# Optimization experiments

Hardware: AMD Instinct MI355X
Metric: run time of the kernel (lower is better)

Reference implementation:

```python
import jax, jax.numpy as jnp
import numpy as np

N_NODES = 8192
N_EDGES = 65536
NB = 10            # number_of_basis
MID = 32           # middle_layer_size
MAX_R = 10.0       # max_radius
NZ, NM = 48, 16    # z / mol embedding sizes -> 64x0e node input
IN_S = NZ + NM     # 64 scalars
H_S, H_V = 32, 8   # hidden irreps 32x0e + 8x1o (dim 56)
O_S = 16           # output irreps 16x0e
W0N = IN_S * H_S + IN_S * H_V                                  # 2560
W1N = H_S*H_S + H_V*H_S + H_S*H_V + H_V*H_V + H_V*H_V          # 1664
W2N = H_S*O_S + H_V*O_S                                        # 640
H_DIM = H_S + 3 * H_V                                          # 56


def _fcnet(e, W1, W2):
    # e3nn FullyConnectedNet([NB, MID, numel], silu): fan-in normalized linears
    h = jax.nn.silu(e @ W1 / np.sqrt(W1.shape[0]))
    return h @ W2 / np.sqrt(W2.shape[0])


def _ln(x, g, b):
    m = jnp.mean(x, -1, keepdims=True)
    v = jnp.var(x, -1, keepdims=True)
    return (x - m) * jax.lax.rsqrt(v + 1e-5) * g + b


def _sus(t):
    # smooth compact-support bump helper: exp(-1/t) for t>0 else 0
    return jnp.where(t > 0, jnp.exp(-1.0 / jnp.where(t > 0, t, 1.0)), 0.0)


def _forward(pos, Ez, Em,
             b0_W1, b0_W2, b0_g, b0_b,
             b1_W1, b1_W2, b1_g, b1_b,
             b2_W1, b2_W2, b2_g, b2_b,
             z, mol_id, edge_src, edge_dst):
    N = pos.shape[0]
    E = edge_src.shape[0]
    avg = E / N  # avg_num_neighbors (static)

    # node embedding: 64x0e
    x = jnp.concatenate([Ez[z], Em[mol_id]], axis=-1)          # [N, 64]

    vec = pos[edge_dst] - pos[edge_src]                        # [E, 3]
    length = jnp.linalg.norm(vec, axis=1)                      # [E]

    # soft_one_hot_linspace(basis='smooth_finite', cutoff=True) * sqrt(NB)
    vals = jnp.linspace(0.0, MAX_R, NB + 2)[1:-1]
    step = MAX_R / (NB + 1)
    u = (length[:, None] - vals) / step
    emb = (1.14136 * np.exp(2.0)) * _sus(u + 1.0) * _sus(1.0 - u)
    emb = emb * np.sqrt(NB)                                    # [E, NB]

    # spherical harmonics lmax=1, normalize=True, 'component' norm
    nrm = vec / jnp.maximum(length, 1e-9)[:, None]
    sh_v = np.sqrt(3.0) * nrm                                  # [E, 3]  (l=1; l=0 comp == 1)

    # ---- interaction block 0: 64x0e -> 32x0e + 8x1o ----
    w = _fcnet(emb, b0_W1, b0_W2)                              # [E, 2560]
    w00 = w[:, :IN_S * H_S].reshape(E, IN_S, H_S)
    w01 = w[:, IN_S * H_S:].reshape(E, IN_S, H_V)
    xe = x[edge_src]                                           # [E, 64]
    es = jnp.einsum('eu,euw->ew', xe, w00) / np.sqrt(IN_S)
    ev = jnp.einsum('eu,euw,ei->ewi', xe, w01, sh_v) / np.sqrt(IN_S)
    msg = jnp.concatenate([es, ev.reshape(E, 3 * H_V)], -1)    # [E, 56]
    x = _ln(jax.ops.segment_sum(msg, edge_dst, num_segments=N) / np.sqrt(avg), b0_g, b0_b)

    # ---- interaction block 1: 32x0e+8x1o -> 32x0e+8x1o ----
    w = _fcnet(emb, b1_W1, b1_W2)                              # [E, 1664]
    o = 0
    w_ss  = w[:, o:o + H_S*H_S].reshape(E, H_S, H_S); o += H_S*H_S
    w_vvs = w[:, o:o + H_V*H_S].reshape(E, H_V, H_S); o += H_V*H_S
    w_sv  = w[:, o:o + H_S*H_V].reshape(E, H_S, H_V); o += H_S*H_V
    w_vs  = w[:, o:o + H_V*H_V].reshape(E, H_V, H_V); o += H_V*H_V
    w_vvv = w[:, o:o + H_V*H_V].reshape(E, H_V, H_V)
    xs = x[:, :H_S][edge_src]                                  # [E, 32]
    xv = x[:, H_S:].reshape(N, H_V, 3)[edge_src]               # [E, 8, 3]
    dot = jnp.einsum('eui,ei->eu', xv, sh_v) / np.sqrt(3.0)    # 1o x 1o -> 0e CG
    crs = jnp.cross(xv, sh_v[:, None, :]) / np.sqrt(2.0)       # 1o x 1o -> 1o CG
    es = (jnp.einsum('eu,euw->ew', xs, w_ss) / np.sqrt(H_S)
          + jnp.einsum('eu,euw->ew', dot, w_vvs) / np.sqrt(H_V)) / np.sqrt(2.0)
    ev = (jnp.einsum('eu,euw,ei->ewi', xs, w_sv, sh_v) / np.sqrt(H_S)
          + jnp.einsum('eui,euw->ewi', xv, w_vs) / np.sqrt(H_V)
          + jnp.einsum('eui,euw->ewi', crs, w_vvv) / np.sqrt(H_V)) / np.sqrt(3.0)
    msg = jnp.concatenate([es, ev.reshape(E, 3 * H_V)], -1)
    x = _ln(jax.ops.segment_sum(msg, edge_dst, num_segments=N) / np.sqrt(avg), b1_g, b1_b)

    # ---- interaction block 2: 32x0e+8x1o -> 16x0e ----
    w = _fcnet(emb, b2_W1, b2_W2)                              # [E, 640]
    w_ss  = w[:, :H_S * O_S].reshape(E, H_S, O_S)
    w_vvs = w[:, H_S * O_S:].reshape(E, H_V, O_S)
    xs = x[:, :H_S][edge_src]
    xv = x[:, H_S:].reshape(N, H_V, 3)[edge_src]
    dot = jnp.einsum('eui,ei->eu', xv, sh_v) / np.sqrt(3.0)
    es = (jnp.einsum('eu,euw->ew', xs, w_ss) / np.sqrt(H_S)
          + jnp.einsum('eu,euw->ew', dot, w_vvs) / np.sqrt(H_V)) / np.sqrt(2.0)
    x = _ln(jax.ops.segment_sum(es, edge_dst, num_segments=N) / np.sqrt(avg), b2_g, b2_b)
    return x                                                   # [N, 16]


def setup_inputs():
    key = jax.random.key(0)
    ks = jax.random.split(key, 16)
    edge_src = jax.random.randint(ks[3], (N_EDGES,), 0, N_NODES)
    # exclude self-loops (radius_graph never returns them)
    edge_dst = (edge_src + 1 + jax.random.randint(ks[4], (N_EDGES,), 0, N_NODES - 1)) % N_NODES
    return {
        'pos': jax.random.uniform(ks[0], (N_NODES, 3), jnp.float32) * 8.0,
        'z': jax.random.randint(ks[1], (N_NODES,), 0, 100),
        'mol_id': jax.random.randint(ks[2], (N_NODES,), 0, 2),
        'edge_src': edge_src,
        'edge_dst': edge_dst,
        'Ez': jax.random.normal(ks[5], (100, NZ), jnp.float32),
        'Em': jax.random.normal(ks[6], (2, NM), jnp.float32),
        'b0_W1': jax.random.normal(ks[7], (NB, MID), jnp.float32),
        'b0_W2': jax.random.normal(ks[8], (MID, W0N), jnp.float32),
        'b0_g': jnp.ones((H_DIM,), jnp.float32),
        'b0_b': jnp.zeros((H_DIM,), jnp.float32),
        'b1_W1': jax.random.normal(ks[9], (NB, MID), jnp.float32),
        'b1_W2': jax.random.normal(ks[10], (MID, W1N), jnp.float32),
        'b1_g': jnp.ones((H_DIM,), jnp.float32),
        'b1_b': jnp.zeros((H_DIM,), jnp.float32),
        'b2_W1': jax.random.normal(ks[11], (NB, MID), jnp.float32),
        'b2_W2': jax.random.normal(ks[12], (MID, W2N), jnp.float32),
        'b2_g': jnp.ones((O_S,), jnp.float32),
        'b2_b': jnp.zeros((O_S,), jnp.float32),
    }


def reference(pos, z, mol_id, edge_src, edge_dst, Ez, Em,
              b0_W1, b0_W2, b0_g, b0_b,
              b1_W1, b1_W2, b1_g, b1_b,
              b2_W1, b2_W2, b2_g, b2_b):
    return _forward(pos, Ez, Em,
                    b0_W1, b0_W2, b0_g, b0_b,
                    b1_W1, b1_W2, b1_g, b1_b,
                    b2_W1, b2_W2, b2_g, b2_b,
                    z, mol_id, edge_src, edge_dst)
```

## Files before the change

### kernel.cpp

```cpp
#include <hip/hip_runtime.h>

#define NNODES 8192
#define NEDGES 65536

#define K_PACK   0.02209708691f
#define K_P1SV   0.01804219593f
#define K_VVS    0.04419417382f
#define K_VS     0.03608439182f
#define K_VVV    0.02551551815f
#define K_DOT    0.57735026919f
#define K_PRELN  0.35355339059f
#define C_EMB    8.4335730689f

typedef unsigned int uint32;
typedef unsigned short ushort16;
typedef __attribute__((ext_vector_type(8))) short short8;
typedef __attribute__((ext_vector_type(4))) float floatx4;

__device__ __forceinline__ float siluf(float x) { return x / (1.0f + __expf(-x)); }
__device__ __forceinline__ float susf(float t) { return t > 0.0f ? __expf(-1.0f / t) : 0.0f; }
__device__ __forceinline__ ushort16 f2bf(float f) {
  uint32 u = __float_as_uint(f);
  return (ushort16)((u + 0x7fffu + ((u >> 16) & 1u)) >> 16);
}
__device__ __forceinline__ float bflo(uint32 v) { return __uint_as_float(v << 16); }
__device__ __forceinline__ float bfhi(uint32 v) { return __uint_as_float(v & 0xffff0000u); }
__device__ __forceinline__ float bfs(ushort16 v) { return __uint_as_float((uint32)v << 16); }

__global__ __launch_bounds__(256) void k_prep(
    const float* __restrict__ pos, const int* __restrict__ z, const int* __restrict__ mol,
    const int* __restrict__ esrc, const int* __restrict__ edst,
    const float* __restrict__ Ez, const float* __restrict__ Em,
    const float* __restrict__ W10, const float* __restrict__ W11, const float* __restrict__ W12,
    const float* __restrict__ W20, const float* __restrict__ W21, const float* __restrict__ W22,
    int* __restrict__ combo, ushort16* __restrict__ X0cb, float* __restrict__ sh,
    ushort16* __restrict__ h0b, ushort16* __restrict__ h1b, ushort16* __restrict__ h2b,
    ushort16* __restrict__ Bp0, ushort16* __restrict__ Bp1, ushort16* __restrict__ Bp2,
    ushort16* __restrict__ Bpw1, ushort16* __restrict__ Bpw2,
    int* __restrict__ deg, int* __restrict__ eidx) {
  __shared__ float Wl[320];
  int b = blockIdx.x;
  if (b < 768) {
    int which = b >> 8;
    int e = ((b & 255) << 8) + threadIdx.x;
    const float* W = (which == 0) ? W10 : (which == 1) ? W11 : W12;
    for (int i = threadIdx.x; i < 320; i += 256) Wl[i] = W[i];
    __syncthreads();
    int s = esrc[e], d = edst[e];
    float vx = pos[d * 3 + 0] - pos[s * 3 + 0];
    float vy = pos[d * 3 + 1] - pos[s * 3 + 1];
    float vz = pos[d * 3 + 2] - pos[s * 3 + 2];
    float len = sqrtf(vx * vx + vy * vy + vz * vz);
    if (which == 0) {
      int p = atomicAdd(&deg[d], 1);
      if (p < 64) eidx[(size_t)d * 64 + p] = e;
      float inv = 1.7320508076f / fmaxf(len, 1e-9f);
      sh[e * 3 + 0] = vx * inv; sh[e * 3 + 1] = vy * inv; sh[e * 3 + 2] = vz * inv;
    }
    float emb[10];
#pragma unroll
    for (int k = 0; k < 10; ++k) {
      float u = len * 1.1f - (float)(k + 1);
      emb[k] = C_EMB * susf(u + 1.0f) * susf(1.0f - u);
    }
    float H[32];
#pragma unroll
    for (int m = 0; m < 32; ++m) {
      float t = 0.f;
#pragma unroll
      for (int k = 0; k < 10; ++k) t += emb[k] * Wl[k * 32 + m];
      H[m] = siluf(t);
    }
    ushort16* hb = (which == 0) ? h0b : (which == 1) ? h1b : h2b;
    uint32* hp = (uint32*)(hb + (size_t)e * 32);
#pragma unroll
    for (int m = 0; m < 16; ++m)
      hp[m] = (uint32)f2bf(H[2 * m]) | ((uint32)f2bf(H[2 * m + 1]) << 16);
    return;
  }
  int idx = (b - 768) * 256 + threadIdx.x;
  if (idx < NNODES) { combo[idx] = z[idx] * 2 + mol[idx]; return; }
  idx -= NNODES;
  if (idx < 16384) {
    int c = idx >> 6, j = idx & 63;
    float v = 0.f;
    if (c < 200) {
      int zz = c >> 1, mm = c & 1;
      v = (j < 48) ? Ez[zz * 48 + j] : Em[mm * 16 + (j - 48)];
    }
    X0cb[idx] = f2bf(v);
    return;
  }
  idx -= 16384;
  if (idx < 81920) {
    int tile = idx >> 10; int r = idx & 1023;
    int kh = r >> 9; int rr = r & 511;
    int lane = rr >> 3, j = rr & 7;
    int k = kh * 32 + (lane >> 4) * 8 + j;
    int n = tile * 16 + (lane & 15);
    int c = n >> 5, m = n & 31;
    int col = (c < 32) ? (k * 32 + c) : (2048 + k * 8 + (c - 32));
    Bp0[idx] = f2bf(W20[m * 2560 + col] * K_PACK);
    return;
  }
  idx -= 81920;
  if (idx < 40960) {
    int tile = idx >> 9; int rr = idx & 511;
    int lane = rr >> 3, j = rr & 7;
    int k = (lane >> 4) * 8 + j;
    int n = tile * 16 + (lane & 15);
    int c = n >> 5, m = n & 31;
    float v = (c < 32) ? W21[m * 1664 + k * 32 + c] * K_PACK
                       : W21[m * 1664 + 1280 + k * 8 + (c - 32)] * K_P1SV;
    Bp1[idx] = f2bf(v);
    return;
  }
  idx -= 40960;
  if (idx < 16384) {
    int tile = idx >> 9; int rr = idx & 511;
    int lane = rr >> 3, j = rr & 7;
    int k = (lane >> 4) * 8 + j;
    int n = tile * 16 + (lane & 15);
    int c = n >> 5, m = n & 31;
    Bp2[idx] = f2bf(W22[m * 640 + k * 16 + c] * K_PACK);
    return;
  }
  idx -= 16384;
  if (idx < 12288) {
    int tile = idx >> 9; int rr = idx & 511;
    int lane = rr >> 3, j = rr & 7;
    int m = (lane >> 4) * 8 + j;
    int c = tile * 16 + (lane & 15);
    float v;
    if (c < 256) {
      int u = c >> 5, w = c & 31;
      v = W21[m * 1664 + 1024 + u * 32 + w] * K_VVS;
    } else {
      int r2 = c - 256; int t = r2 & 1; int l2 = r2 >> 1;
      int u = l2 >> 3, vv = l2 & 7;
      v = (t == 0) ? W21[m * 1664 + 1536 + u * 8 + vv] * K_VS
                   : W21[m * 1664 + 1600 + u * 8 + vv] * K_VVV;
    }
    Bpw1[idx] = f2bf(v);
    return;
  }
  idx -= 12288;
  {
    int tile = idx >> 9; int rr = idx & 511;
    int lane = rr >> 3, j = rr & 7;
    int m = (lane >> 4) * 8 + j;
    int c = tile * 16 + (lane & 15);
    int t = c & 1; int l2 = c >> 1;
    int u = l2 >> 3, wh = l2 & 7;
    Bpw2[idx] = f2bf(W22[m * 640 + 512 + u * 16 + wh * 2 + t] * K_VVS);
  }
}

__device__ __forceinline__ void gemm_tile(
    const ushort16* __restrict__ A, const ushort16* __restrict__ Bp, ushort16* __restrict__ C,
    int N, int K, int bx, int by, int wave, int lane) {
  int m0 = bx * 64 + wave * 16;
  int n0 = by * 64;
  int row = lane & 15, q = lane >> 4;
  int nkh = K >> 5;
  floatx4 acc[4];
  floatx4 zero = {0.f, 0.f, 0.f, 0.f};
#pragma unroll
  for (int t = 0; t < 4; ++t) acc[t] = zero;
  for (int kh = 0; kh < nkh; ++kh) {
    short8 a = *reinterpret_cast<const short8*>(A + (size_t)(m0 + row) * K + kh * 32 + q * 8);
#pragma unroll
    for (int t = 0; t < 4; ++t) {
      int T = (n0 >> 4) + t;
      short8 b = *reinterpret_cast<const short8*>(Bp + ((size_t)T * nkh + kh) * 512 + lane * 8);
      acc[t] = __builtin_amdgcn_mfma_f32_16x16x32_bf16(a, b, acc[t], 0, 0, 0);
    }
  }
  int colb = n0 + row;
#pragma unroll
  for (int t = 0; t < 4; ++t)
#pragma unroll
    for (int r = 0; r < 4; ++r)
      C[(size_t)(m0 + q * 4 + r) * N + colb + t * 16] = f2bf(acc[t][r]);
}

__global__ __launch_bounds__(256) void k_gemm_mfma(
    const ushort16* __restrict__ A, const ushort16* __restrict__ Bp, ushort16* __restrict__ C,
    int N, int K) {
  gemm_tile(A, Bp, C, N, K, blockIdx.x, blockIdx.y, threadIdx.x >> 6, threadIdx.x & 63);
}

__global__ __launch_bounds__(256) void k_msg0(
    const int* __restrict__ rowmap, const int* __restrict__ esrc,
    const float* __restrict__ sh, const ushort16* __restrict__ hb,
    const ushort16* __restrict__ Pb, ushort16* __restrict__ msg) {
  int e = __builtin_amdgcn_readfirstlane(blockIdx.x * 4 + (threadIdx.x >> 6));
  int lane = threadIdx.x & 63;
  int s = esrc[e];
  int row = rowmap[s];
  float sh0 = sh[e * 3 + 0], sh1 = sh[e * 3 + 1], sh2 = sh[e * 3 + 2];
  int c; float mult;
  if (lane < 32) { c = lane; mult = 1.0f; }
  else if (lane < 56) {
    int l = lane - 32; int v = l / 3; int i = l - v * 3;
    c = 32 + v;
    mult = (i == 0) ? sh0 : (i == 1 ? sh1 : sh2);
  } else { c = 0; mult = 0.0f; }
  const uint4* Hp = reinterpret_cast<const uint4*>(hb + (size_t)e * 32);
  const uint4* Pp = reinterpret_cast<const uint4*>(Pb + (size_t)row * 1280 + c * 32);
  float a = 0.f;
#pragma unroll
  for (int qq = 0; qq < 4; ++qq) {
    uint4 pv = Pp[qq];
    uint4 hv = Hp[qq];
    a += bflo(pv.x) * bflo(hv.x) + bfhi(pv.x) * bfhi(hv.x);
    a += bflo(pv.y) * bflo(hv.y) + bfhi(pv.y) * bfhi(hv.y);
    a += bflo(pv.z) * bflo(hv.z) + bfhi(pv.z) * bfhi(hv.z);
    a += bflo(pv.w) * bflo(hv.w) + bfhi(pv.w) * bfhi(hv.w);
  }
  if (lane < 56) msg[(size_t)e * 56 + lane] = f2bf(a * mult);
}

__global__ __launch_bounds__(256) void k_msg1f(
    const int* __restrict__ esrc, const float* __restrict__ sh, const ushort16* __restrict__ hb,
    const ushort16* __restrict__ Pb, const float* __restrict__ xv,
    const ushort16* __restrict__ Bpw, ushort16* __restrict__ msg) {
  __shared__ ushort16 Wlds[16][384];
  __shared__ float vbuf[4][56];
  int w = threadIdx.x >> 6, lane = threadIdx.x & 63;
  int e0 = __builtin_amdgcn_readfirstlane(blockIdx.x * 16);
  int row = lane & 15, q = lane >> 4;
  short8 a1 = *reinterpret_cast<const short8*>(hb + (size_t)(e0 + row) * 32 + q * 8);
  floatx4 zero = {0.f, 0.f, 0.f, 0.f};
#pragma unroll
  for (int t6 = 0; t6 < 6; ++t6) {
    int T = w * 6 + t6;
    short8 b1 = *reinterpret_cast<const short8*>(Bpw + (size_t)T * 512 + lane * 8);
    floatx4 acc = __builtin_amdgcn_mfma_f32_16x16x32_bf16(a1, b1, zero, 0, 0, 0);
#pragma unroll
    for (int r = 0; r < 4; ++r)
      Wlds[q * 4 + r][T * 16 + row] = f2bf(acc[r]);
  }
  __syncthreads();
  int u = lane >> 3;
#pragma unroll
  for (int k = 0; k < 4; ++k) {
    int e = e0 + w * 4 + k;
    int s = esrc[e];
    float sh0 = sh[e * 3 + 0], sh1 = sh[e * 3 + 1], sh2 = sh[e * 3 + 2];
    const float* xvp = xv + (size_t)s * 24 + u * 3;
    float x0 = xvp[0], x1 = xvp[1], x2 = xvp[2];
    float du = K_DOT * (x0 * sh0 + x1 * sh1 + x2 * sh2);
    float cr0 = x1 * sh2 - x2 * sh1;
    float cr1 = x2 * sh0 - x0 * sh2;
    float cr2 = x0 * sh1 - x1 * sh0;
    const ushort16* wp = &Wlds[w * 4 + k][0];
    uint2 wv = *reinterpret_cast<const uint2*>(wp + lane * 4);
    uint32 wsv = *reinterpret_cast<const uint32*>(wp + 256 + lane * 2);
    float b0 = du * bflo(wv.x), b1 = du * bfhi(wv.x);
    float b2 = du * bflo(wv.y), b3 = du * bfhi(wv.y);
    float avs = bflo(wsv), avv = bfhi(wsv);
    float e0v = x0 * avs + cr0 * avv;
    float e1v = x1 * avs + cr1 * avv;
    float e2v = x2 * avs + cr2 * avv;
#pragma unroll
    for (int off = 8; off < 64; off <<= 1) {
      b0 += __shfl_xor(b0, off, 64); b1 += __shfl_xor(b1, off, 64);
      b2 += __shfl_xor(b2, off, 64); b3 += __shfl_xor(b3, off, 64);
      e0v += __shfl_xor(e0v, off, 64); e1v += __shfl_xor(e1v, off, 64);
      e2v += __shfl_xor(e2v, off, 64);
    }
    if (lane < 8) {
      vbuf[w][lane * 4 + 0] = b0; vbuf[w][lane * 4 + 1] = b1;
      vbuf[w][lane * 4 + 2] = b2; vbuf[w][lane * 4 + 3] = b3;
      vbuf[w][32 + lane * 3 + 0] = e0v;
      vbuf[w][32 + lane * 3 + 1] = e1v;
      vbuf[w][32 + lane * 3 + 2] = e2v;
    }
    int c; float mult;
    if (lane < 32) { c = lane; mult = 1.0f; }
    else if (lane < 56) {
      int l = lane - 32; int v = l / 3; int i = l - v * 3;
      c = 32 + v;
      mult = (i == 0) ? sh0 : (i == 1 ? sh1 : sh2);
    } else { c = 0; mult = 0.0f; }
    const uint4* Hp = reinterpret_cast<const uint4*>(hb + (size_t)e * 32);
    const uint4* Pp = reinterpret_cast<const uint4*>(Pb + (size_t)s * 1280 + c * 32);
    float a = 0.f;
#pragma unroll
    for (int qq = 0; qq < 4; ++qq) {
      uint4 pv = Pp[qq];
      uint4 hv = Hp[qq];
      a += bflo(pv.x) * bflo(hv.x) + bfhi(pv.x) * bfhi(hv.x);
      a += bflo(pv.y) * bflo(hv.y) + bfhi(pv.y) * bfhi(hv.y);
      a += bflo(pv.z) * bflo(hv.z) + bfhi(pv.z) * bfhi(hv.z);
      a += bflo(pv.w) * bflo(hv.w) + bfhi(pv.w) * bfhi(hv.w);
    }
    __syncthreads();
    if (lane < 56) msg[(size_t)e * 56 + lane] = f2bf(a * mult + vbuf[w][lane]);
  }
}

__global__ __launch_bounds__(256) void k_msg2f(
    const int* __restrict__ esrc, const float* __restrict__ sh, const ushort16* __restrict__ hb,
    const ushort16* __restrict__ Pb, const float* __restrict__ xv,
    const ushort16* __restrict__ Bpw, ushort16* __restrict__ msg) {
  __shared__ ushort16 Wlds[16][128];
  __shared__ float vbuf[4][16];
  int w = threadIdx.x >> 6, lane = threadIdx.x & 63;
  int e0 = __builtin_amdgcn_readfirstlane(blockIdx.x * 16);
  int row = lane & 15, q = lane >> 4;
  short8 a1 = *reinterpret_cast<const short8*>(hb + (size_t)(e0 + row) * 32 + q * 8);
  floatx4 zero = {0.f, 0.f, 0.f, 0.f};
#pragma unroll
  for (int t2 = 0; t2 < 2; ++t2) {
    int T = w * 2 + t2;
    short8 b1 = *reinterpret_cast<const short8*>(Bpw + (size_t)T * 512 + lane * 8);
    floatx4 acc = __builtin_amdgcn_mfma_f32_16x16x32_bf16(a1, b1, zero, 0, 0, 0);
#pragma unroll
    for (int r = 0; r < 4; ++r)
      Wlds[q * 4 + r][T * 16 + row] = f2bf(acc[r]);
  }
  __syncthreads();
  int u = lane >> 3;
#pragma unroll
  for (int k = 0; k < 4; ++k) {
    int e = e0 + w * 4 + k;
    int s = esrc[e];
    float sh0 = sh[e * 3 + 0], sh1 = sh[e * 3 + 1], sh2 = sh[e * 3 + 2];
    const float* xvp = xv + (size_t)s * 24 + u * 3;
    float du = K_DOT * (xvp[0] * sh0 + xvp[1] * sh1 + xvp[2] * sh2);
    uint32 w2 = *reinterpret_cast<const uint32*>(&Wlds[w * 4 + k][0] + lane * 2);
    float c0 = du * bflo(w2), c1 = du * bfhi(w2);
#pragma unroll
    for (int off = 8; off < 64; off <<= 1) {
      c0 += __shfl_xor(c0, off, 64); c1 += __shfl_xor(c1, off, 64);
    }
    if (lane < 8) { vbuf[w][lane * 2 + 0] = c0; vbuf[w][lane * 2 + 1] = c1; }
    int qq = lane >> 4, wc = lane & 15;
    uint4 hv = reinterpret_cast<const uint4*>(hb + (size_t)e * 32)[qq];
    uint4 pv = reinterpret_cast<const uint4*>(Pb + (size_t)s * 512 + wc * 32)[qq];
    float a = bflo(pv.x) * bflo(hv.x) + bfhi(pv.x) * bfhi(hv.x)
            + bflo(pv.y) * bflo(hv.y) + bfhi(pv.y) * bfhi(hv.y)
            + bflo(pv.z) * bflo(hv.z) + bfhi(pv.z) * bfhi(hv.z)
            + bflo(pv.w) * bflo(hv.w) + bfhi(pv.w) * bfhi(hv.w);
    a += __shfl_xor(a, 16, 64);
    a += __shfl_xor(a, 32, 64);
    __syncthreads();
    if (lane < 16) msg[(size_t)e * 16 + lane] = f2bf(a + vbuf[w][lane]);
  }
}

__global__ __launch_bounds__(256) void k_gather_ln(
    const int* __restrict__ deg, const int* __restrict__ eidx,
    const ushort16* __restrict__ msg, int D,
    const float* __restrict__ g, const float* __restrict__ b,
    ushort16* __restrict__ xsb, float* __restrict__ xvf, float* __restrict__ outf) {
  int n = __builtin_amdgcn_readfirstlane(blockIdx.x * 4 + (threadIdx.x >> 6));
  int lane = threadIdx.x & 63;
  int cnt = deg[n]; if (cnt > 64) cnt = 64;
  const int* ep = eidx + (size_t)n * 64;
  float v = 0.f;
  for (int j = 0; j < cnt; ++j) {
    int e = ep[j];
    if (lane < D) v += bfs(msg[(size_t)e * D + lane]);
  }
  v *= K_PRELN;
  if (lane >= D) v = 0.f;
  float sm = v, sq = v * v;
#pragma unroll
  for (int off = 32; off > 0; off >>= 1) {
    sm += __shfl_xor(sm, off, 64);
    sq += __shfl_xor(sq, off, 64);
  }
  float invD = 1.0f / (float)D;
  float mean = sm * invD;
  float var = sq * invD - mean * mean;
  float rs = rsqrtf(var + 1e-5f);
  float r = (v - mean) * rs * g[lane < D ? lane : 0] + b[lane < D ? lane : 0];
  if (outf) {
    if (lane < D) outf[(size_t)n * D + lane] = r;
  } else {
    if (lane < 32) xsb[(size_t)n * 32 + lane] = f2bf(r);
    else if (lane < 56) xvf[(size_t)n * 24 + lane - 32] = r;
  }
}

extern "C" void kernel_launch(void* const* d_in, const int* in_sizes, int n_in,
                              void* d_out, int out_size, void* d_ws, size_t ws_size,
                              hipStream_t stream) {
  const float* pos = (const float*)d_in[0];
  const int* z = (const int*)d_in[1];
  const int* mol = (const int*)d_in[2];
  const int* esrc = (const int*)d_in[3];
  const int* edst = (const int*)d_in[4];
  const float* Ez = (const float*)d_in[5];
  const float* Em = (const float*)d_in[6];
  const float* b0W1 = (const float*)d_in[7];
  const float* b0W2 = (const float*)d_in[8];
  const float* b0g = (const float*)d_in[9];
  const float* b0b = (const float*)d_in[10];
  const float* b1W1 = (const float*)d_in[11];
  const float* b1W2 = (const float*)d_in[12];
  const float* b1g = (const float*)d_in[13];
  const float* b1b = (const float*)d_in[14];
  const float* b2W1 = (const float*)d_in[15];
  const float* b2W2 = (const float*)d_in[16];
  const float* b2g = (const float*)d_in[17];
  const float* b2b = (const float*)d_in[18];
  float* out = (float*)d_out;

  float* ws = (float*)d_ws;
  size_t o = 0;
  int* combo = (int*)(ws + o); o += NNODES;
  int* deg = (int*)(ws + o); o += NNODES;
  int* eidx = (int*)(ws + o); o += (size_t)NNODES * 64;
  ushort16* X0cb = (ushort16*)(ws + o); o += 8192;
  ushort16* xs1b = (ushort16*)(ws + o); o += 131072;
  float* xv1 = ws + o; o += (size_t)NNODES * 24;
  ushort16* h0b = (ushort16*)(ws + o); o += (size_t)NEDGES * 16;
  ushort16* h1b = (ushort16*)(ws + o); o += (size_t)NEDGES * 16;
  ushort16* h2b = (ushort16*)(ws + o); o += (size_t)NEDGES * 16;
  float* shb = ws + o; o += (size_t)NEDGES * 3;
  ushort16* Bp0 = (ushort16*)(ws + o); o += 40960;
  ushort16* Bp1 = (ushort16*)(ws + o); o += 20480;
  ushort16* Bp2 = (ushort16*)(ws + o); o += 8192;
  ushort16* Bpw1 = (ushort16*)(ws + o); o += 6144;
  ushort16* Bpw2 = (ushort16*)(ws + o); o += 2048;
  ushort16* P12 = (ushort16*)(ws + o); o += (size_t)NNODES * 640;
  ushort16* msgb = (ushort16*)(ws + o); o += (size_t)NEDGES * 28;

  ushort16* P0c = P12;
  ushort16* xs2b = xs1b;
  float* xv2 = xv1;
  ushort16* msg16 = msgb;

  hipMemsetAsync(deg, 0, NNODES * sizeof(int), stream);

  k_prep<<<1472, 256, 0, stream>>>(pos, z, mol, esrc, edst, Ez, Em,
                                   b0W1, b1W1, b2W1, b0W2, b1W2, b2W2,
                                   combo, X0cb, shb, h0b, h1b, h2b,
                                   Bp0, Bp1, Bp2, Bpw1, Bpw2, deg, eidx);

  k_gemm_mfma<<<dim3(4, 20), 256, 0, stream>>>(X0cb, Bp0, P0c, 1280, 64);
  k_msg0<<<16384, 256, 0, stream>>>(combo, esrc, shb, h0b, P0c, msgb);
  k_gather_ln<<<2048, 256, 0, stream>>>(deg, eidx, msgb, 56, b0g, b0b, xs1b, xv1, nullptr);

  k_gemm_mfma<<<dim3(128, 20), 256, 0, stream>>>(xs1b, Bp1, P12, 1280, 32);
  k_msg1f<<<4096, 256, 0, stream>>>(esrc, shb, h1b, P12, xv1, Bpw1, msgb);
  k_gather_ln<<<2048, 256, 0, stream>>>(deg, eidx, msgb, 56, b1g, b1b, xs2b, xv2, nullptr);

  k_gemm_mfma<<<dim3(128, 8), 256, 0, stream>>>(xs2b, Bp2, P12, 512, 32);
  k_msg2f<<<4096, 256, 0, stream>>>(esrc, shb, h2b, P12, xv2, Bpw2, msg16);
  k_gather_ln<<<2048, 256, 0, stream>>>(deg, eidx, msg16, 16, b2g, b2b, nullptr, nullptr, out);
}
```

Before: 225.0 us.

## Process edges in source-sorted order for message kernels with block swizzle

Counts out-degree per source node, scans it into row pointers (fused into the first GEMM launch), and builds a source-sorted edge permutation during k_msg0. k_msg1f and k_msg2f then walk edges in that permuted order, so consecutive edges share the same source-node P rows and xv data. They also use a block-index swizzle. The aim is better L2 locality for the per-source gathers. The cost is extra atomics, a scan and indirect edge indexing. Messages are still written by original edge id, so the gather stage is unchanged.

```diff
diff --git a/kernel.cpp b/kernel.cpp
--- a/kernel.cpp
+++ b/kernel.cpp
@@ -37,7 +37,7 @@
     ushort16* __restrict__ h0b, ushort16* __restrict__ h1b, ushort16* __restrict__ h2b,
     ushort16* __restrict__ Bp0, ushort16* __restrict__ Bp1, ushort16* __restrict__ Bp2,
     ushort16* __restrict__ Bpw1, ushort16* __restrict__ Bpw2,
-    int* __restrict__ deg, int* __restrict__ eidx) {
+    int* __restrict__ deg, int* __restrict__ deg_s, int* __restrict__ eidx) {
   __shared__ float Wl[320];
   int b = blockIdx.x;
   if (b < 768) {
@@ -54,6 +54,7 @@
     if (which == 0) {
       int p = atomicAdd(&deg[d], 1);
       if (p < 64) eidx[(size_t)d * 64 + p] = e;
+      atomicAdd(&deg_s[s], 1);
       float inv = 1.7320508076f / fmaxf(len, 1e-9f);
       sh[e * 3 + 0] = vx * inv; sh[e * 3 + 1] = vy * inv; sh[e * 3 + 2] = vz * inv;
     }
@@ -190,13 +191,47 @@
   gemm_tile(A, Bp, C, N, K, blockIdx.x, blockIdx.y, threadIdx.x >> 6, threadIdx.x & 63);
 }
 
+__global__ __launch_bounds__(256) void k_gemm_scan(
+    const ushort16* __restrict__ A, const ushort16* __restrict__ Bp, ushort16* __restrict__ C,
+    const int* __restrict__ deg_s, int* __restrict__ rowptr_s) {
+  __shared__ int sums[256];
+  int b = blockIdx.x;
+  if (b < 80) {
+    gemm_tile(A, Bp, C, 1280, 64, b % 4, b / 4, threadIdx.x >> 6, threadIdx.x & 63);
+    return;
+  }
+  int t = threadIdx.x;
+  int base = t * 32;
+  int local[32];
+  int s = 0;
+#pragma unroll
+  for (int i = 0; i < 32; ++i) { local[i] = s; s += deg_s[base + i]; }
+  sums[t] = s;
+  __syncthreads();
+  for (int off = 1; off < 256; off <<= 1) {
+    int v = (t >= off) ? sums[t - off] : 0;
+    __syncthreads();
+    sums[t] += v;
+    __syncthreads();
+  }
+  int prev = (t == 0) ? 0 : sums[t - 1];
+#pragma unroll
+  for (int i = 0; i < 32; ++i) rowptr_s[base + i] = prev + local[i];
+  if (t == 255) rowptr_s[NNODES] = sums[255];
+}
+
 __global__ __launch_bounds__(256) void k_msg0(
     const int* __restrict__ rowmap, const int* __restrict__ esrc,
     const float* __restrict__ sh, const ushort16* __restrict__ hb,
-    const ushort16* __restrict__ Pb, ushort16* __restrict__ msg) {
+    const ushort16* __restrict__ Pb, ushort16* __restrict__ msg,
+    const int* __restrict__ rowptr_s, int* __restrict__ fill_s, int* __restrict__ eperm) {
   int e = __builtin_amdgcn_readfirstlane(blockIdx.x * 4 + (threadIdx.x >> 6));
   int lane = threadIdx.x & 63;
   int s = esrc[e];
+  if (lane == 0) {
+    int p = atomicAdd(&fill_s[s], 1);
+    eperm[rowptr_s[s] + p] = e;
+  }
   int row = rowmap[s];
   float sh0 = sh[e * 3 + 0], sh1 = sh[e * 3 + 1], sh2 = sh[e * 3 + 2];
   int c; float mult;
@@ -222,15 +257,19 @@
 }
 
 __global__ __launch_bounds__(256) void k_msg1f(
-    const int* __restrict__ esrc, const float* __restrict__ sh, const ushort16* __restrict__ hb,
+    const int* __restrict__ eperm, const int* __restrict__ esrc,
+    const float* __restrict__ sh, const ushort16* __restrict__ hb,
     const ushort16* __restrict__ Pb, const float* __restrict__ xv,
     const ushort16* __restrict__ Bpw, ushort16* __restrict__ msg) {
   __shared__ ushort16 Wlds[16][384];
   __shared__ float vbuf[4][56];
   int w = threadIdx.x >> 6, lane = threadIdx.x & 63;
-  int e0 = __builtin_amdgcn_readfirstlane(blockIdx.x * 16);
+  int bid = blockIdx.x;
+  int swz = (bid & 7) * 512 + (bid >> 3);
+  int e0 = __builtin_amdgcn_readfirstlane(swz * 16);
   int row = lane & 15, q = lane >> 4;
-  short8 a1 = *reinterpret_cast<const short8*>(hb + (size_t)(e0 + row) * 32 + q * 8);
+  int er = eperm[e0 + row];
+  short8 a1 = *reinterpret_cast<const short8*>(hb + (size_t)er * 32 + q * 8);
   floatx4 zero = {0.f, 0.f, 0.f, 0.f};
 #pragma unroll
   for (int t6 = 0; t6 < 6; ++t6) {
@@ -245,7 +284,7 @@
   int u = lane >> 3;
 #pragma unroll
   for (int k = 0; k < 4; ++k) {
-    int e = e0 + w * 4 + k;
+    int e = __builtin_amdgcn_readfirstlane(eperm[e0 + w * 4 + k]);
     int s = esrc[e];
     float sh0 = sh[e * 3 + 0], sh1 = sh[e * 3 + 1], sh2 = sh[e * 3 + 2];
     const float* xvp = xv + (size_t)s * 24 + u * 3;
@@ -302,15 +341,19 @@
 }
 
 __global__ __launch_bounds__(256) void k_msg2f(
-    const int* __restrict__ esrc, const float* __restrict__ sh, const ushort16* __restrict__ hb,
+    const int* __restrict__ eperm, const int* __restrict__ esrc,
+    const float* __restrict__ sh, const ushort16* __restrict__ hb,
     const ushort16* __restrict__ Pb, const float* __restrict__ xv,
     const ushort16* __restrict__ Bpw, ushort16* __restrict__ msg) {
   __shared__ ushort16 Wlds[16][128];
   __shared__ float vbuf[4][16];
   int w = threadIdx.x >> 6, lane = threadIdx.x & 63;
-  int e0 = __builtin_amdgcn_readfirstlane(blockIdx.x * 16);
+  int bid = blockIdx.x;
+  int swz = (bid & 7) * 512 + (bid >> 3);
+  int e0 = __builtin_amdgcn_readfirstlane(swz * 16);
   int row = lane & 15, q = lane >> 4;
-  short8 a1 = *reinterpret_cast<const short8*>(hb + (size_t)(e0 + row) * 32 + q * 8);
+  int er = eperm[e0 + row];
+  short8 a1 = *reinterpret_cast<const short8*>(hb + (size_t)er * 32 + q * 8);
   floatx4 zero = {0.f, 0.f, 0.f, 0.f};
 #pragma unroll
   for (int t2 = 0; t2 < 2; ++t2) {
@@ -325,7 +368,7 @@
   int u = lane >> 3;
 #pragma unroll
   for (int k = 0; k < 4; ++k) {
-    int e = e0 + w * 4 + k;
+    int e = __builtin_amdgcn_readfirstlane(eperm[e0 + w * 4 + k]);
     int s = esrc[e];
     float sh0 = sh[e * 3 + 0], sh1 = sh[e * 3 + 1], sh2 = sh[e * 3 + 2];
     const float* xvp = xv + (size_t)s * 24 + u * 3;
@@ -414,6 +457,10 @@
   size_t o = 0;
   int* combo = (int*)(ws + o); o += NNODES;
   int* deg = (int*)(ws + o); o += NNODES;
+  int* deg_s = (int*)(ws + o); o += NNODES;
+  int* fill_s = (int*)(ws + o); o += NNODES;
+  int* rowptr_s = (int*)(ws + o); o += NNODES + 8;
+  int* eperm = (int*)(ws + o); o += NEDGES;
   int* eidx = (int*)(ws + o); o += (size_t)NNODES * 64;
   ushort16* X0cb = (ushort16*)(ws + o); o += 8192;
   ushort16* xs1b = (ushort16*)(ws + o); o += 131072;
@@ -435,22 +482,23 @@
   float* xv2 = xv1;
   ushort16* msg16 = msgb;
 
-  hipMemsetAsync(deg, 0, NNODES * sizeof(int), stream);
+  hipMemsetAsync(deg, 0, 3 * NNODES * sizeof(int), stream);
 
   k_prep<<<1472, 256, 0, stream>>>(pos, z, mol, esrc, edst, Ez, Em,
                                    b0W1, b1W1, b2W1, b0W2, b1W2, b2W2,
                                    combo, X0cb, shb, h0b, h1b, h2b,
-                                   Bp0, Bp1, Bp2, Bpw1, Bpw2, deg, eidx);
-
-  k_gemm_mfma<<<dim3(4, 20), 256, 0, stream>>>(X0cb, Bp0, P0c, 1280, 64);
-  k_msg0<<<16384, 256, 0, stream>>>(combo, esrc, shb, h0b, P0c, msgb);
+                                   Bp0, Bp1, Bp2, Bpw1, Bpw2, deg, deg_s, eidx);
+
+  k_gemm_scan<<<81, 256, 0, stream>>>(X0cb, Bp0, P0c, deg_s, rowptr_s);
+  k_msg0<<<16384, 256, 0, stream>>>(combo, esrc, shb, h0b, P0c, msgb,
+                                    rowptr_s, fill_s, eperm);
   k_gather_ln<<<2048, 256, 0, stream>>>(deg, eidx, msgb, 56, b0g, b0b, xs1b, xv1, nullptr);
 
   k_gemm_mfma<<<dim3(128, 20), 256, 0, stream>>>(xs1b, Bp1, P12, 1280, 32);
-  k_msg1f<<<4096, 256, 0, stream>>>(esrc, shb, h1b, P12, xv1, Bpw1, msgb);
+  k_msg1f<<<4096, 256, 0, stream>>>(eperm, esrc, shb, h1b, P12, xv1, Bpw1, msgb);
   k_gather_ln<<<2048, 256, 0, stream>>>(deg, eidx, msgb, 56, b1g, b1b, xs2b, xv2, nullptr);
 
   k_gemm_mfma<<<dim3(128, 8), 256, 0, stream>>>(xs2b, Bp2, P12, 512, 32);
-  k_msg2f<<<4096, 256, 0, stream>>>(esrc, shb, h2b, P12, xv2, Bpw2, msg16);
+  k_msg2f<<<4096, 256, 0, stream>>>(eperm, esrc, shb, h2b, P12, xv2, Bpw2, msg16);
   k_gather_ln<<<2048, 256, 0, stream>>>(deg, eidx, msg16, 16, b2g, b2b, nullptr, nullptr, out);
 }
```

Result: slower. 229.8 us (+2.2%).
